# Kernel tuning notes

Hardware: AMD Instinct MI355X
Metric: run time of the kernel (lower is better)

The kernel has to match this reference:

```python
import jax, jax.numpy as jnp
import numpy as np

B, V, K, DIN, H, DH, OBS, HID = 2048, 3, 32, 256, 8, 64, 128, 256
REP = H * DH
EPS = 1e-6


def _ln(x, g, b):
    mu = x.mean(-1, keepdims=True)
    var = ((x - mu) ** 2).mean(-1, keepdims=True)
    return (x - mu) * jax.lax.rsqrt(var + 1e-5) * g + b


def setup_inputs() -> dict:
    key = jax.random.key(0)
    ks = iter(jax.random.split(key, 32))
    nrm = lambda shape, s=0.05: jax.random.normal(next(ks), shape, jnp.float32) * s
    return {
        'x_anchor': jax.random.normal(next(ks), (B, V, DIN), jnp.float32),
        'x_neighbors': jax.random.normal(next(ks), (B, V, K, DIN), jnp.float32),
        'edge_weights': jax.random.uniform(next(ks), (B, V, K), jnp.float32),
        'g': jax.random.normal(next(ks), (B, OBS), jnp.float32),
        'aW': nrm((V, DIN, REP)), 'ab': jnp.zeros((V, REP)), 'ag': jnp.ones((V, REP)), 'abeta': jnp.zeros((V, REP)),
        'nW': nrm((V, DIN, REP)), 'nb': jnp.zeros((V, REP)), 'ng': jnp.ones((V, REP)), 'nbeta': jnp.zeros((V, REP)),
        'Wq': nrm((V, H, DH, DH)), 'Wk': nrm((V, H, DH, DH)), 'Wv': nrm((V, H, DH, DH)), 'Wo': nrm((V, H, DH, DH)),
        'geom_log_scale': jnp.zeros((V, H)),
        'cWq': nrm((H, DH, DH)), 'cWk': nrm((H, DH, DH)), 'cWv': nrm((H, DH, DH)), 'cWo': nrm((H, DH, DH)),
        'rW1': nrm((OBS, HID)), 'rb1': jnp.zeros((HID,)),
        'rW2': nrm((HID, HID)), 'rb2': jnp.zeros((HID,)),
        'vW': nrm((HID, H * V)), 'vb': jnp.zeros((H * V,)),
        'mW': nrm((HID, H)), 'mb': jnp.zeros((H,)),
        'gW': nrm((HID, H)), 'gb': jnp.zeros((H,)),
    }


def reference(x_anchor, x_neighbors, edge_weights, g, aW, ab, ag, abeta, nW, nb, ng, nbeta,
              Wq, Wk, Wv, Wo, geom_log_scale, cWq, cWk, cWv, cWo,
              rW1, rb1, rW2, rb2, vW, vb, mW, mb, gW, gb):
    # --- per-view encoders (vectorized over V with a leading v axis) ---
    ha = _ln(jnp.einsum('bvi,vio->bvo', x_anchor, aW) + ab, ag, abeta).reshape(B, V, H, DH)
    hn = _ln(jnp.einsum('bvki,vio->bvko', x_neighbors, nW) + nb[:, None, :],
             ng[:, None, :], nbeta[:, None, :]).reshape(B, V, K, H, DH)
    q = jnp.einsum('bvhd,vhde->bvhe', ha, Wq)
    k = jnp.einsum('bvkhd,vhde->bvkhe', hn, Wk)
    vv = jnp.einsum('bvkhd,vhde->bvkhe', hn, Wv)
    sc = jnp.einsum('bvhd,bvkhd->bvhk', q, k) / np.sqrt(DH).astype(np.float32)
    geom = jax.nn.softplus(geom_log_scale)  # [V,H]
    sc = sc + geom[None, :, :, None] * jnp.log(edge_weights[:, :, None, :] + EPS)
    attn = jax.nn.softmax(sc, axis=-1)
    ho = jnp.einsum('bvhk,bvkhd->bvhd', attn, vv)
    ho = jnp.einsum('bvhd,vhde->bvhe', ho, Wo) + ha  # residual
    view_tokens = jnp.transpose(ho, (0, 2, 1, 3))  # [B,H,V,Dh]
    # --- router ---
    hid = jax.nn.gelu(jnp.dot(g, rW1) + rb1, approximate=False)
    hid = jax.nn.gelu(jnp.dot(hid, rW2) + rb2, approximate=False)
    pi = jax.nn.softmax((jnp.dot(hid, vW) + vb).reshape(B, H, V), axis=-1)
    beta = jax.nn.sigmoid((jnp.dot(hid, mW) + mb)[..., None])  # [B,H,1]
    gate = jax.nn.softmax(jnp.dot(hid, gW) + gb, axis=-1)      # [B,H]
    # --- pi-weighted mixture + cross-view interaction with log-pi prior ---
    mix = jnp.einsum('bhv,bhvd->bhd', pi, view_tokens)
    qc = jnp.einsum('bhd,hde->bhe', mix, cWq)
    kc = jnp.einsum('bhvd,hde->bhve', view_tokens, cWk)
    vc = jnp.einsum('bhvd,hde->bhve', view_tokens, cWv)
    s2 = jnp.einsum('bhd,bhvd->bhv', qc, kc) / np.sqrt(DH).astype(np.float32) + jnp.log(pi + EPS)
    a2 = jax.nn.softmax(s2, axis=-1)
    cr = jnp.einsum('bhv,bhvd->bhd', a2, vc)
    cr = jnp.einsum('bhd,hde->bhe', cr, cWo)
    # mode blend + head gating; head_repr kept unflattened [B,H,Dh]
    return gate[..., None] * (beta * cr + (1.0 - beta) * mix)
```

## Files before the change

### kernel.cpp

```cpp
#include <hip/hip_runtime.h>

#define B_   2048
#define V_   3
#define K_   32
#define DIN_ 256
#define H_   8
#define DH_  64
#define REP_ 512

typedef unsigned short u16;
typedef unsigned int   u32;
typedef __bf16 bf8 __attribute__((ext_vector_type(8)));
typedef float  f4  __attribute__((ext_vector_type(4)));

static __device__ __forceinline__ u16 f2bf(float f) {
  union { float f; u32 i; } x; x.f = f;
  u32 r = (x.i + 0x7FFFu + ((x.i >> 16) & 1u)) >> 16;
  return (u16)r;
}
static __device__ __forceinline__ float bf2f(u16 u) {
  union { u32 i; float f; } x; x.i = ((u32)u) << 16;
  return x.f;
}

static __device__ __forceinline__ void gl2lds16(const u16* g, u16* l) {
  __builtin_amdgcn_global_load_lds(
      (const __attribute__((address_space(1))) unsigned int*)(g),
      (__attribute__((address_space(3))) unsigned int*)(l), 16, 0, 0);
}
#define ASYNC_BARRIER() asm volatile("s_waitcnt vmcnt(0)\n\ts_barrier" ::: "memory")

__global__ __launch_bounds__(256) void k0_prep(
    const float* __restrict__ nW, const float* __restrict__ aW,
    const float* __restrict__ Wk, const float* __restrict__ Wv,
    u16* __restrict__ nWt, u16* __restrict__ aWt,
    u16* __restrict__ Wkt, u16* __restrict__ Wvt)
{
  int id = blockIdx.x * 256 + threadIdx.x;
  if (id < 393216) {
    int v  = id / 131072, r  = id % 131072;
    int kt = r / 16384,   r2 = r % 16384;
    int n  = r2 >> 5;
    int s  = (r2 >> 3) & 3;
    int m  = r2 & 7;
    int c  = s ^ ((n >> 1) & 3);
    int k  = kt * 32 + c * 8 + m;
    int src = (v * 256 + k) * 512 + n;
    nWt[id] = f2bf(nW[src]);
    aWt[id] = f2bf(aW[src]);
  } else {
    int j = id - 393216;
    int vh = j / 4096, r = j % 4096;
    int e = r / 64, d = r % 64;
    int src = (vh * 64 + d) * 64 + e;
    Wkt[j] = f2bf(Wk[src]);
    Wvt[j] = f2bf(Wv[src]);
  }
}

__global__ __launch_bounds__(256, 2) void k1_gemm_ln(
    const float* __restrict__ X,
    const u16*   __restrict__ Wt,
    const float* __restrict__ bias,
    const float* __restrict__ gamma,
    const float* __restrict__ betap,
    u16*   __restrict__ hn,
    float* __restrict__ ha,
    int mode, int b0, int Bc)
{
  __shared__ u16 sA[32 * 256];
  __shared__ u16 sB[2][16384];
  const int v = blockIdx.y, blk = blockIdx.x, t = threadIdx.x;
  const int w = t >> 6, l = t & 63, lm = l & 15, lg = l >> 4;

  float bcol[8];
  #pragma unroll
  for (int tn = 0; tn < 8; ++tn) bcol[tn] = bias[v * 512 + w * 128 + tn * 16 + lm];

  {
    int row = t >> 3;
    int cbase = (t & 7) * 32;
    long grow;
    if (mode == 0) { int b = b0 + blk; grow = ((long)(b * 3 + v) * 32 + row) * 256; }
    else           { int b = blk * 32 + row; grow = (long)(b * 3 + v) * 256; }
    const float4* src = (const float4*)(X + grow + cbase);
    int sw = row & 7;
    #pragma unroll
    for (int j = 0; j < 8; ++j) {
      float4 f = src[j];
      int col = cbase + j * 4;
      int c = col >> 3, m = col & 7;
      ushort4 u;
      u.x = f2bf(f.x); u.y = f2bf(f.y); u.z = f2bf(f.z); u.w = f2bf(f.w);
      *(ushort4*)&sA[row * 256 + ((c ^ sw) << 3) + m] = u;
    }
  }

  const u16* Wbase = Wt + (long)v * 8 * 16384;
  {
    const u16* gp = Wbase + w * 4096 + l * 8;
    u16* lp = &sB[0][w * 4096];
    #pragma unroll
    for (int j = 0; j < 8; ++j) gl2lds16(gp + j * 512, lp + j * 512);
  }
  __syncthreads();

  f4 acc[2][8];
  #pragma unroll
  for (int i = 0; i < 2; ++i)
    #pragma unroll
    for (int j = 0; j < 8; ++j) { f4 z = {0.f, 0.f, 0.f, 0.f}; acc[i][j] = z; }

  #pragma unroll
  for (int kt = 0; kt < 8; ++kt) {
    if (kt < 7) {
      const u16* gp = Wbase + (kt + 1) * 16384 + w * 4096 + l * 8;
      u16* lp = &sB[(kt + 1) & 1][w * 4096];
      #pragma unroll
      for (int j = 0; j < 8; ++j) gl2lds16(gp + j * 512, lp + j * 512);
    }
    const u16* Bcur = &sB[kt & 1][0];
    bf8 af[2];
    #pragma unroll
    for (int tm = 0; tm < 2; ++tm) {
      int row = tm * 16 + lm;
      int c = kt * 4 + lg;
      af[tm] = *(const bf8*)&sA[row * 256 + ((c ^ (row & 7)) << 3)];
    }
    #pragma unroll
    for (int tn = 0; tn < 8; ++tn) {
      int n = w * 128 + tn * 16 + lm;
      bf8 bv = *(const bf8*)&Bcur[n * 32 + ((lg ^ ((n >> 1) & 3)) << 3)];
      acc[0][tn] = __builtin_amdgcn_mfma_f32_16x16x32_bf16(af[0], bv, acc[0][tn], 0, 0, 0);
      acc[1][tn] = __builtin_amdgcn_mfma_f32_16x16x32_bf16(af[1], bv, acc[1][tn], 0, 0, 0);
    }
    if (kt < 7) ASYNC_BARRIER();
  }
  __syncthreads();

  u16* S = &sB[0][0];
  #pragma unroll
  for (int tm = 0; tm < 2; ++tm)
    #pragma unroll
    for (int tn = 0; tn < 8; ++tn) {
      int col = w * 128 + tn * 16 + lm;
      int c = col >> 3, m = col & 7;
      #pragma unroll
      for (int r = 0; r < 4; ++r) {
        int row = tm * 16 + lg * 4 + r;
        S[row * 512 + ((c ^ (row & 7)) << 3) + m] = f2bf(acc[tm][tn][r] + bcol[tn]);
      }
    }
  __syncthreads();

  {
    int row = t >> 3, ch = t & 7, sw = row & 7;
    float s1 = 0.f, s2 = 0.f;
    #pragma unroll
    for (int j = 0; j < 8; ++j) {
      int c = j * 8 + ch;
      const u16* p8 = &S[row * 512 + ((c ^ sw) << 3)];
      #pragma unroll
      for (int m = 0; m < 8; ++m) { float x = bf2f(p8[m]); s1 += x; s2 += x * x; }
    }
    #pragma unroll
    for (int d = 1; d < 8; d <<= 1) { s1 += __shfl_xor(s1, d, 64); s2 += __shfl_xor(s2, d, 64); }
    float mu = s1 * (1.f / 512.f);
    float var = s2 * (1.f / 512.f) - mu * mu;
    float rs = rsqrtf(var + 1e-5f);
    #pragma unroll
    for (int j = 0; j < 8; ++j) {
      int c = j * 8 + ch;
      const u16* p8 = &S[row * 512 + ((c ^ sw) << 3)];
      int col0 = c * 8;
      float4 g0 = *(const float4*)&gamma[v * 512 + col0];
      float4 g1 = *(const float4*)&gamma[v * 512 + col0 + 4];
      float4 e0 = *(const float4*)&betap[v * 512 + col0];
      float4 e1 = *(const float4*)&betap[v * 512 + col0 + 4];
      float y0 = (bf2f(p8[0]) - mu) * rs * g0.x + e0.x;
      float y1 = (bf2f(p8[1]) - mu) * rs * g0.y + e0.y;
      float y2 = (bf2f(p8[2]) - mu) * rs * g0.z + e0.z;
      float y3 = (bf2f(p8[3]) - mu) * rs * g0.w + e0.w;
      float y4 = (bf2f(p8[4]) - mu) * rs * g1.x + e1.x;
      float y5 = (bf2f(p8[5]) - mu) * rs * g1.y + e1.y;
      float y6 = (bf2f(p8[6]) - mu) * rs * g1.z + e1.z;
      float y7 = (bf2f(p8[7]) - mu) * rs * g1.w + e1.w;
      if (mode == 0) {
        uint4 q4;
        q4.x = (u32)f2bf(y0) | ((u32)f2bf(y1) << 16);
        q4.y = (u32)f2bf(y2) | ((u32)f2bf(y3) << 16);
        q4.z = (u32)f2bf(y4) | ((u32)f2bf(y5) << 16);
        q4.w = (u32)f2bf(y6) | ((u32)f2bf(y7) << 16);
        u16* dst = hn + (((long)(v * 8 + j) * Bc + blk) * 32 + row) * 64 + ch * 8;
        *(uint4*)dst = q4;
      } else {
        int b = blk * 32 + row;
        float* dst = ha + (long)(b * 3 + v) * 512 + col0;
        float4 w0, w1;
        w0.x = y0; w0.y = y1; w0.z = y2; w0.w = y3;
        w1.x = y4; w1.y = y5; w1.z = y6; w1.w = y7;
        *(float4*)dst = w0;
        *(float4*)(dst + 4) = w1;
      }
    }
  }
}

__global__ __launch_bounds__(256, 2) void k2_attn(
    const u16*   __restrict__ hn,
    const float* __restrict__ ha,
    const u16*   __restrict__ Wkt,
    const u16*   __restrict__ Wvt,
    const float* __restrict__ Wq,
    const float* __restrict__ Wo,
    const float* __restrict__ ew,
    const float* __restrict__ gls,
    float* __restrict__ vt,
    int b0, int Bc)
{
  const int v = blockIdx.z, h = blockIdx.y;
  const int bL0 = blockIdx.x * 4;
  const int t = threadIdx.x;
  __shared__ u16 A[128 * 72];
  __shared__ u16 Wk_s[64 * 72], Wv_s[64 * 72];
  __shared__ float q_s[4 * 64], ha_s[4 * 64], attn_s[4 * 32], o_s[4 * 64];

  {
    const uint4* src = (const uint4*)(hn + ((long)(v * 8 + h) * Bc + bL0) * 2048);
    int r = t >> 1, half = t & 1;
    #pragma unroll
    for (int i = 0; i < 4; ++i) {
      uint4 d = src[r * 8 + half * 4 + i];
      *(uint4*)&A[r * 72 + half * 32 + i * 8] = d;
    }
  }
  {
    const uint4* sk = (const uint4*)(Wkt + (long)(v * 8 + h) * 4096);
    const uint4* sv = (const uint4*)(Wvt + (long)(v * 8 + h) * 4096);
    #pragma unroll
    for (int i = 0; i < 2; ++i) {
      int idx = i * 256 + t;
      int n = idx >> 3, k8 = (idx & 7) * 8;
      *(uint4*)&Wk_s[n * 72 + k8] = sk[idx];
      *(uint4*)&Wv_s[n * 72 + k8] = sv[idx];
    }
  }
  {
    int b = t >> 6, e = t & 63;
    ha_s[t] = ha[((long)(b0 + bL0 + b) * 3 + v) * 512 + h * 64 + e];
  }
  __syncthreads();

  const int w = t >> 6, l = t & 63, lm = l & 15, lg = l >> 4;
  f4 aK[2][4], aV[2][4];
  #pragma unroll
  for (int i = 0; i < 2; ++i)
    #pragma unroll
    for (int j = 0; j < 4; ++j) { f4 z = {0.f, 0.f, 0.f, 0.f}; aK[i][j] = z; aV[i][j] = z; }

  #pragma unroll
  for (int ks = 0; ks < 2; ++ks) {
    int ko = ks * 32 + lg * 8;
    bf8 af[2];
    #pragma unroll
    for (int tm = 0; tm < 2; ++tm) af[tm] = *(const bf8*)&A[(w * 32 + tm * 16 + lm) * 72 + ko];
    #pragma unroll
    for (int tn = 0; tn < 4; ++tn) {
      bf8 bk = *(const bf8*)&Wk_s[(tn * 16 + lm) * 72 + ko];
      bf8 bv = *(const bf8*)&Wv_s[(tn * 16 + lm) * 72 + ko];
      #pragma unroll
      for (int tm = 0; tm < 2; ++tm) {
        aK[tm][tn] = __builtin_amdgcn_mfma_f32_16x16x32_bf16(af[tm], bk, aK[tm][tn], 0, 0, 0);
        aV[tm][tn] = __builtin_amdgcn_mfma_f32_16x16x32_bf16(af[tm], bv, aV[tm][tn], 0, 0, 0);
      }
    }
  }
  __syncthreads();

  #pragma unroll
  for (int tm = 0; tm < 2; ++tm)
    #pragma unroll
    for (int tn = 0; tn < 4; ++tn)
      #pragma unroll
      for (int r = 0; r < 4; ++r) {
        int row = w * 32 + tm * 16 + lg * 4 + r;
        int col = tn * 16 + lm;
        A[row * 72 + col] = f2bf(aK[tm][tn][r]);
      }
  {
    const float* wq = Wq + (long)(v * 8 + h) * 4096;
    int b = t >> 6, e = t & 63;
    float acc = 0.f;
    for (int d = 0; d < 64; ++d) acc += ha_s[b * 64 + d] * wq[d * 64 + e];
    q_s[t] = acc * 0.125f;
  }
  __syncthreads();

  if (t < 128) {
    int b = t >> 5, k = t & 31;
    float x = gls[v * 8 + h];
    float gsc = (x > 20.f) ? x : log1pf(expf(x));
    float s = 0.f;
    const u16* kr = &A[(b * 32 + k) * 72];
    for (int d = 0; d < 64; ++d) s += q_s[b * 64 + d] * bf2f(kr[d]);
    float e_w = ew[((long)(b0 + bL0 + b) * 3 + v) * 32 + k];
    s += gsc * logf(e_w + 1e-6f);
    float m = s;
    #pragma unroll
    for (int d = 1; d < 32; d <<= 1) m = fmaxf(m, __shfl_xor(m, d, 64));
    float exs = expf(s - m), sum = exs;
    #pragma unroll
    for (int d = 1; d < 32; d <<= 1) sum += __shfl_xor(sum, d, 64);
    attn_s[b * 32 + k] = exs / sum;
  }
  __syncthreads();

  {
    float p[4] = {0.f, 0.f, 0.f, 0.f};
    #pragma unroll
    for (int tm = 0; tm < 2; ++tm)
      #pragma unroll
      for (int r = 0; r < 4; ++r) {
        int k = tm * 16 + lg * 4 + r;
        float a = attn_s[w * 32 + k];
        #pragma unroll
        for (int tn = 0; tn < 4; ++tn) p[tn] += a * aV[tm][tn][r];
      }
    #pragma unroll
    for (int tn = 0; tn < 4; ++tn) {
      float x = p[tn];
      x += __shfl_xor(x, 16, 64);
      x += __shfl_xor(x, 32, 64);
      if (l < 16) o_s[w * 64 + tn * 16 + lm] = x;
    }
  }
  __syncthreads();

  {
    const float* wo = Wo + (long)(v * 8 + h) * 4096;
    int b = t >> 6, e = t & 63;
    float acc = ha_s[b * 64 + e];
    for (int d = 0; d < 64; ++d) acc += o_s[b * 64 + d] * wo[d * 64 + e];
    vt[(((long)(b0 + bL0 + b) * 8 + h) * 3 + v) * 64 + e] = acc;
  }
}

__global__ __launch_bounds__(256) void k3_router(
    const float* __restrict__ g, const float* __restrict__ rW1, const float* __restrict__ rb1,
    const float* __restrict__ rW2, const float* __restrict__ rb2,
    const float* __restrict__ vW, const float* __restrict__ vb,
    const float* __restrict__ mW, const float* __restrict__ mb,
    const float* __restrict__ gW, const float* __restrict__ gb,
    float* __restrict__ pi, float* __restrict__ beta_o, float* __restrict__ gate_o)
{
  __shared__ float gs[4 * 128], h1[4 * 256], h2[4 * 256], lgt[4 * 40];
  int t = threadIdx.x, bb = blockIdx.x * 4;
  #pragma unroll
  for (int r = 0; r < 2; ++r) { int idx = r * 256 + t; gs[idx] = g[(long)bb * 128 + idx]; }
  __syncthreads();
  {
    int bl = t >> 6, e0 = (t & 63) * 4;
    float acc[4];
    #pragma unroll
    for (int j = 0; j < 4; ++j) acc[j] = rb1[e0 + j];
    for (int i = 0; i < 128; ++i) {
      float gv = gs[bl * 128 + i];
      const float* wr = rW1 + i * 256 + e0;
      #pragma unroll
      for (int j = 0; j < 4; ++j) acc[j] += gv * wr[j];
    }
    #pragma unroll
    for (int j = 0; j < 4; ++j) { float x = acc[j]; h1[bl * 256 + e0 + j] = 0.5f * x * (1.f + erff(x * 0.70710678118f)); }
  }
  __syncthreads();
  {
    int bl = t >> 6, e0 = (t & 63) * 4;
    float acc[4];
    #pragma unroll
    for (int j = 0; j < 4; ++j) acc[j] = rb2[e0 + j];
    for (int i = 0; i < 256; ++i) {
      float hv = h1[bl * 256 + i];
      const float* wr = rW2 + i * 256 + e0;
      #pragma unroll
      for (int j = 0; j < 4; ++j) acc[j] += hv * wr[j];
    }
    #pragma unroll
    for (int j = 0; j < 4; ++j) { float x = acc[j]; h2[bl * 256 + e0 + j] = 0.5f * x * (1.f + erff(x * 0.70710678118f)); }
  }
  __syncthreads();
  if (t < 160) {
    int bl = t / 40, j = t % 40;
    const float* W; float bs; int col, stride;
    if (j < 24)      { W = vW; col = j;      stride = 24; bs = vb[j]; }
    else if (j < 32) { W = mW; col = j - 24; stride = 8;  bs = mb[j - 24]; }
    else             { W = gW; col = j - 32; stride = 8;  bs = gb[j - 32]; }
    float acc = bs;
    for (int i = 0; i < 256; ++i) acc += h2[bl * 256 + i] * W[i * stride + col];
    lgt[bl * 40 + j] = acc;
  }
  __syncthreads();
  if (t < 4) {
    int b = bb + t;
    const float* L = &lgt[t * 40];
    #pragma unroll
    for (int hh = 0; hh < 8; ++hh) {
      float a0 = L[hh * 3], a1 = L[hh * 3 + 1], a2v = L[hh * 3 + 2];
      float m = fmaxf(a0, fmaxf(a1, a2v));
      float x0 = expf(a0 - m), x1 = expf(a1 - m), x2 = expf(a2v - m);
      float inv = 1.f / (x0 + x1 + x2);
      pi[b * 24 + hh * 3 + 0] = x0 * inv;
      pi[b * 24 + hh * 3 + 1] = x1 * inv;
      pi[b * 24 + hh * 3 + 2] = x2 * inv;
      beta_o[b * 8 + hh] = 1.f / (1.f + expf(-L[24 + hh]));
    }
    float m = L[32];
    #pragma unroll
    for (int hh = 1; hh < 8; ++hh) m = fmaxf(m, L[32 + hh]);
    float s = 0.f, ex[8];
    #pragma unroll
    for (int hh = 0; hh < 8; ++hh) { ex[hh] = expf(L[32 + hh] - m); s += ex[hh]; }
    float inv = 1.f / s;
    #pragma unroll
    for (int hh = 0; hh < 8; ++hh) gate_o[b * 8 + hh] = ex[hh] * inv;
  }
}

__global__ __launch_bounds__(256) void k4_cross(
    const float* __restrict__ vtg, const float* __restrict__ pig,
    const float* __restrict__ betag, const float* __restrict__ gateg,
    const float* __restrict__ cWq, const float* __restrict__ cWk,
    const float* __restrict__ cWv, const float* __restrict__ cWo,
    float* __restrict__ out)
{
  __shared__ float smem[12544];
  float* vts   = smem;
  float* mixs  = smem + 6144;
  float* buf1  = smem + 8192;
  float* buf2  = smem + 10240;
  float* a2s   = smem + 12288;
  float* pis   = smem + 12384;
  float* betas = smem + 12480;
  float* gates = smem + 12512;

  int t = threadIdx.x, bblk = blockIdx.x * 4;
  {
    const float4* src = (const float4*)(vtg + (long)bblk * 1536);
    #pragma unroll
    for (int r = 0; r < 6; ++r) ((float4*)vts)[r * 256 + t] = src[r * 256 + t];
    if (t < 96) pis[t] = pig[bblk * 24 + t];
    if (t < 32) { betas[t] = betag[bblk * 8 + t]; gates[t] = gateg[bblk * 8 + t]; }
  }
  __syncthreads();
  int bl = t >> 6, hh = (t >> 3) & 7, e0 = (t & 7) * 8;
  const float* vbh = &vts[(bl * 8 + hh) * 192];
  {
    float p0 = pis[bl * 24 + hh * 3], p1 = pis[bl * 24 + hh * 3 + 1], p2 = pis[bl * 24 + hh * 3 + 2];
    #pragma unroll
    for (int j = 0; j < 8; ++j) {
      int e = e0 + j;
      mixs[(bl * 8 + hh) * 64 + e] = p0 * vbh[e] + p1 * vbh[64 + e] + p2 * vbh[128 + e];
    }
  }
  __syncthreads();
  {
    float acc[8] = {0.f,0.f,0.f,0.f,0.f,0.f,0.f,0.f};
    const float* M = &mixs[(bl * 8 + hh) * 64];
    for (int d = 0; d < 64; ++d) {
      float mv = M[d];
      const float* wr = &cWq[(hh * 64 + d) * 64 + e0];
      #pragma unroll
      for (int j = 0; j < 8; ++j) acc[j] += mv * wr[j];
    }
    #pragma unroll
    for (int j = 0; j < 8; ++j) buf1[(bl * 8 + hh) * 64 + e0 + j] = acc[j] * 0.125f;
  }
  __syncthreads();
  {
    const float* Q = &buf1[(bl * 8 + hh) * 64];
    #pragma unroll
    for (int d2 = 0; d2 < 8; ++d2) {
      const float* wr = &cWk[(hh * 64 + e0 + d2) * 64];
      float a = 0.f;
      for (int e = 0; e < 64; ++e) a += wr[e] * Q[e];
      buf2[(bl * 8 + hh) * 64 + e0 + d2] = a;
    }
  }
  __syncthreads();
  if (t < 32) {
    int b2 = t >> 3, h2 = t & 7;
    const float* Wd = &buf2[(b2 * 8 + h2) * 64];
    const float* vb2 = &vts[(b2 * 8 + h2) * 192];
    float s[3];
    #pragma unroll
    for (int v3 = 0; v3 < 3; ++v3) {
      float a = 0.f;
      for (int d = 0; d < 64; ++d) a += Wd[d] * vb2[v3 * 64 + d];
      s[v3] = a + logf(pis[b2 * 24 + h2 * 3 + v3] + 1e-6f);
    }
    float m = fmaxf(s[0], fmaxf(s[1], s[2]));
    float x0 = expf(s[0] - m), x1 = expf(s[1] - m), x2 = expf(s[2] - m);
    float inv = 1.f / (x0 + x1 + x2);
    a2s[(b2 * 8 + h2) * 3 + 0] = x0 * inv;
    a2s[(b2 * 8 + h2) * 3 + 1] = x1 * inv;
    a2s[(b2 * 8 + h2) * 3 + 2] = x2 * inv;
  }
  __syncthreads();
  {
    float a0 = a2s[(bl * 8 + hh) * 3], a1 = a2s[(bl * 8 + hh) * 3 + 1], a2v = a2s[(bl * 8 + hh) * 3 + 2];
    #pragma unroll
    for (int j = 0; j < 8; ++j) {
      int e = e0 + j;
      buf1[(bl * 8 + hh) * 64 + e] = a0 * vbh[e] + a1 * vbh[64 + e] + a2v * vbh[128 + e];
    }
  }
  __syncthreads();
  {
    float acc[8] = {0.f,0.f,0.f,0.f,0.f,0.f,0.f,0.f};
    const float* Y = &buf1[(bl * 8 + hh) * 64];
    for (int d = 0; d < 64; ++d) {
      float yv = Y[d];
      const float* wr = &cWv[(hh * 64 + d) * 64 + e0];
      #pragma unroll
      for (int j = 0; j < 8; ++j) acc[j] += yv * wr[j];
    }
    #pragma unroll
    for (int j = 0; j < 8; ++j) buf2[(bl * 8 + hh) * 64 + e0 + j] = acc[j];
  }
  __syncthreads();
  {
    float acc[8] = {0.f,0.f,0.f,0.f,0.f,0.f,0.f,0.f};
    const float* C2 = &buf2[(bl * 8 + hh) * 64];
    for (int d = 0; d < 64; ++d) {
      float cv = C2[d];
      const float* wr = &cWo[(hh * 64 + d) * 64 + e0];
      #pragma unroll
      for (int j = 0; j < 8; ++j) acc[j] += cv * wr[j];
    }
    float bt = betas[bl * 8 + hh], gt = gates[bl * 8 + hh];
    const float* M = &mixs[(bl * 8 + hh) * 64];
    #pragma unroll
    for (int j = 0; j < 8; ++j)
      out[((long)(bblk + bl) * 8 + hh) * 64 + e0 + j] = gt * (bt * acc[j] + (1.f - bt) * M[e0 + j]);
  }
}

extern "C" void kernel_launch(void* const* d_in, const int* in_sizes, int n_in,
                              void* d_out, int out_size, void* d_ws, size_t ws_size,
                              hipStream_t stream) {
  const float* x_anchor    = (const float*)d_in[0];
  const float* x_neighbors = (const float*)d_in[1];
  const float* edge_w      = (const float*)d_in[2];
  const float* g           = (const float*)d_in[3];
  const float* aW  = (const float*)d_in[4];
  const float* ab  = (const float*)d_in[5];
  const float* ag  = (const float*)d_in[6];
  const float* abeta = (const float*)d_in[7];
  const float* nW  = (const float*)d_in[8];
  const float* nb  = (const float*)d_in[9];
  const float* ng  = (const float*)d_in[10];
  const float* nbeta = (const float*)d_in[11];
  const float* Wq  = (const float*)d_in[12];
  const float* Wk  = (const float*)d_in[13];
  const float* Wv  = (const float*)d_in[14];
  const float* Wo  = (const float*)d_in[15];
  const float* gls = (const float*)d_in[16];
  const float* cWq = (const float*)d_in[17];
  const float* cWk = (const float*)d_in[18];
  const float* cWv = (const float*)d_in[19];
  const float* cWo = (const float*)d_in[20];
  const float* rW1 = (const float*)d_in[21];
  const float* rb1 = (const float*)d_in[22];
  const float* rW2 = (const float*)d_in[23];
  const float* rb2 = (const float*)d_in[24];
  const float* vW  = (const float*)d_in[25];
  const float* vb  = (const float*)d_in[26];
  const float* mW  = (const float*)d_in[27];
  const float* mb  = (const float*)d_in[28];
  const float* gW  = (const float*)d_in[29];
  const float* gb  = (const float*)d_in[30];

  char* p = (char*)d_ws;
  u16* nWt = (u16*)p;  p += 786432;
  u16* aWt = (u16*)p;  p += 786432;
  u16* Wkt = (u16*)p;  p += 196608;
  u16* Wvt = (u16*)p;  p += 196608;
  float* ha   = (float*)p; p += 12582912;
  float* vtb  = (float*)p; p += 12582912;
  float* pib  = (float*)p; p += 196608;
  float* betb = (float*)p; p += 65536;
  float* gatb = (float*)p; p += 65536;
  size_t fixed = (size_t)(p - (char*)d_ws);
  int C = 1;
  while (C < 128 && fixed + (size_t)(2048 / C) * 98304 > ws_size) C <<= 1;
  int Bc = 2048 / C;
  u16* hnb = (u16*)p;

  k0_prep<<<1920, 256, 0, stream>>>(nW, aW, Wk, Wv, nWt, aWt, Wkt, Wvt);
  k1_gemm_ln<<<dim3(64, 3), 256, 0, stream>>>(x_anchor, aWt, ab, ag, abeta,
                                              (u16*)nullptr, ha, 1, 0, Bc);
  k3_router<<<512, 256, 0, stream>>>(g, rW1, rb1, rW2, rb2, vW, vb, mW, mb, gW, gb,
                                     pib, betb, gatb);
  for (int c = 0; c < C; ++c) {
    int b0 = c * Bc;
    k1_gemm_ln<<<dim3(Bc, 3), 256, 0, stream>>>(x_neighbors, nWt, nb, ng, nbeta,
                                                hnb, (float*)nullptr, 0, b0, Bc);
    k2_attn<<<dim3(Bc / 4, 8, 3), 256, 0, stream>>>(hnb, ha, Wkt, Wvt, Wq, Wo,
                                                    edge_w, gls, vtb, b0, Bc);
  }
  k4_cross<<<512, 256, 0, stream>>>(vtb, pib, betb, gatb, cWq, cWk, cWv, cWo,
                                    (float*)d_out);
}
```

Baseline: 784.7 us.

## Fold Wq·Wk^T into one matrix, enlarge GEMM-LN tile to 64 rows

Precomputes Wqk = Wq·Wk^T per view-head, so attention scores come from ha·Wqk dotted directly with hn. This removes the K projection MFMAs, the LDS round trip of K, and the Wk staging in the attention kernel. The neighbor GEMM+LayerNorm kernel now runs 512 threads per block over 64 rows, reusing each weight tile across twice as many rows, but it drops the double-buffered async weight prefetch for a single buffer with two barriers per k-step. The LN and score loops also read bf16 values as packed 128-bit words.

Result: faster. 748.6 us (-4.6%).

```diff
diff --git a/kernel.cpp b/kernel.cpp
--- a/kernel.cpp
+++ b/kernel.cpp
@@ -22,19 +22,24 @@
   union { u32 i; float f; } x; x.i = ((u32)u) << 16;
   return x.f;
 }
+static __device__ __forceinline__ float bflo(u32 q) {
+  union { u32 i; float f; } x; x.i = q << 16; return x.f;
+}
+static __device__ __forceinline__ float bfhi(u32 q) {
+  union { u32 i; float f; } x; x.i = q & 0xffff0000u; return x.f;
+}
 
 static __device__ __forceinline__ void gl2lds16(const u16* g, u16* l) {
   __builtin_amdgcn_global_load_lds(
       (const __attribute__((address_space(1))) unsigned int*)(g),
       (__attribute__((address_space(3))) unsigned int*)(l), 16, 0, 0);
 }
-#define ASYNC_BARRIER() asm volatile("s_waitcnt vmcnt(0)\n\ts_barrier" ::: "memory")
 
 __global__ __launch_bounds__(256) void k0_prep(
     const float* __restrict__ nW, const float* __restrict__ aW,
-    const float* __restrict__ Wk, const float* __restrict__ Wv,
+    const float* __restrict__ Wv,
     u16* __restrict__ nWt, u16* __restrict__ aWt,
-    u16* __restrict__ Wkt, u16* __restrict__ Wvt)
+    u16* __restrict__ Wvt)
 {
   int id = blockIdx.x * 256 + threadIdx.x;
   if (id < 393216) {
@@ -53,12 +58,44 @@
     int vh = j / 4096, r = j % 4096;
     int e = r / 64, d = r % 64;
     int src = (vh * 64 + d) * 64 + e;
-    Wkt[j] = f2bf(Wk[src]);
     Wvt[j] = f2bf(Wv[src]);
   }
 }
 
-__global__ __launch_bounds__(256, 2) void k1_gemm_ln(
+__global__ __launch_bounds__(256) void k0_wqk(
+    const float* __restrict__ Wq, const float* __restrict__ Wk,
+    float* __restrict__ Wqk)
+{
+  int vh = blockIdx.x, t = threadIdx.x;
+  __shared__ float wq[4096], wkT[4096];
+  #pragma unroll
+  for (int i = 0; i < 16; ++i) {
+    int idx = i * 256 + t;
+    wq[idx] = Wq[(long)vh * 4096 + idx];
+    int e = idx >> 6, c = idx & 63;
+    wkT[c * 64 + e] = Wk[(long)vh * 4096 + e * 64 + c];
+  }
+  __syncthreads();
+  int d = t >> 2, e0 = (t & 3) * 16;
+  float acc[16];
+  #pragma unroll
+  for (int j = 0; j < 16; ++j) acc[j] = 0.f;
+  for (int c = 0; c < 64; ++c) {
+    float a = wq[d * 64 + c];
+    const float* wr = &wkT[c * 64 + e0];
+    #pragma unroll
+    for (int j = 0; j < 16; ++j) acc[j] += a * wr[j];
+  }
+  #pragma unroll
+  for (int j = 0; j < 16; ++j) Wqk[(long)vh * 4096 + d * 64 + e0 + j] = acc[j];
+}
+
+union K1Smem {
+  struct { u16 A[64 * 256]; u16 B[16384]; } p;
+  u16 S[64 * 512];
+};
+
+__global__ __launch_bounds__(512, 4) void k1_gemm_ln(
     const float* __restrict__ X,
     const u16*   __restrict__ Wt,
     const float* __restrict__ bias,
@@ -68,21 +105,21 @@
     float* __restrict__ ha,
     int mode, int b0, int Bc)
 {
-  __shared__ u16 sA[32 * 256];
-  __shared__ u16 sB[2][16384];
+  __shared__ K1Smem sm;
   const int v = blockIdx.y, blk = blockIdx.x, t = threadIdx.x;
   const int w = t >> 6, l = t & 63, lm = l & 15, lg = l >> 4;
+  const int wm = w & 1, wn = w >> 1;
 
   float bcol[8];
   #pragma unroll
-  for (int tn = 0; tn < 8; ++tn) bcol[tn] = bias[v * 512 + w * 128 + tn * 16 + lm];
+  for (int tn = 0; tn < 8; ++tn) bcol[tn] = bias[v * 512 + wn * 128 + tn * 16 + lm];
 
   {
     int row = t >> 3;
     int cbase = (t & 7) * 32;
     long grow;
-    if (mode == 0) { int b = b0 + blk; grow = ((long)(b * 3 + v) * 32 + row) * 256; }
-    else           { int b = blk * 32 + row; grow = (long)(b * 3 + v) * 256; }
+    if (mode == 0) { int b = b0 + blk * 2 + (row >> 5); grow = ((long)(b * 3 + v) * 32 + (row & 31)) * 256; }
+    else           { int b = blk * 64 + row;            grow = (long)(b * 3 + v) * 256; }
     const float4* src = (const float4*)(X + grow + cbase);
     int sw = row & 7;
     #pragma unroll
@@ -92,63 +129,53 @@
       int c = col >> 3, m = col & 7;
       ushort4 u;
       u.x = f2bf(f.x); u.y = f2bf(f.y); u.z = f2bf(f.z); u.w = f2bf(f.w);
-      *(ushort4*)&sA[row * 256 + ((c ^ sw) << 3) + m] = u;
-    }
-  }
+      *(ushort4*)&sm.p.A[row * 256 + ((c ^ sw) << 3) + m] = u;
+    }
+  }
+
+  f4 acc[2][8];
+  #pragma unroll
+  for (int i = 0; i < 2; ++i)
+    #pragma unroll
+    for (int j = 0; j < 8; ++j) { f4 z = {0.f, 0.f, 0.f, 0.f}; acc[i][j] = z; }
 
   const u16* Wbase = Wt + (long)v * 8 * 16384;
-  {
-    const u16* gp = Wbase + w * 4096 + l * 8;
-    u16* lp = &sB[0][w * 4096];
-    #pragma unroll
-    for (int j = 0; j < 8; ++j) gl2lds16(gp + j * 512, lp + j * 512);
-  }
-  __syncthreads();
-
-  f4 acc[2][8];
-  #pragma unroll
-  for (int i = 0; i < 2; ++i)
-    #pragma unroll
-    for (int j = 0; j < 8; ++j) { f4 z = {0.f, 0.f, 0.f, 0.f}; acc[i][j] = z; }
-
-  #pragma unroll
   for (int kt = 0; kt < 8; ++kt) {
-    if (kt < 7) {
-      const u16* gp = Wbase + (kt + 1) * 16384 + w * 4096 + l * 8;
-      u16* lp = &sB[(kt + 1) & 1][w * 4096];
-      #pragma unroll
-      for (int j = 0; j < 8; ++j) gl2lds16(gp + j * 512, lp + j * 512);
-    }
-    const u16* Bcur = &sB[kt & 1][0];
+    __syncthreads();
+    {
+      const u16* gp = Wbase + (long)kt * 16384 + t * 8;
+      u16* lp = &sm.p.B[t * 8];
+      #pragma unroll
+      for (int r = 0; r < 4; ++r) gl2lds16(gp + r * 4096, lp + r * 4096);
+    }
+    __syncthreads();
     bf8 af[2];
     #pragma unroll
     for (int tm = 0; tm < 2; ++tm) {
-      int row = tm * 16 + lm;
+      int row = wm * 32 + tm * 16 + lm;
       int c = kt * 4 + lg;
-      af[tm] = *(const bf8*)&sA[row * 256 + ((c ^ (row & 7)) << 3)];
+      af[tm] = *(const bf8*)&sm.p.A[row * 256 + ((c ^ (row & 7)) << 3)];
     }
     #pragma unroll
     for (int tn = 0; tn < 8; ++tn) {
-      int n = w * 128 + tn * 16 + lm;
-      bf8 bv = *(const bf8*)&Bcur[n * 32 + ((lg ^ ((n >> 1) & 3)) << 3)];
+      int n = wn * 128 + tn * 16 + lm;
+      bf8 bv = *(const bf8*)&sm.p.B[n * 32 + ((lg ^ ((n >> 1) & 3)) << 3)];
       acc[0][tn] = __builtin_amdgcn_mfma_f32_16x16x32_bf16(af[0], bv, acc[0][tn], 0, 0, 0);
       acc[1][tn] = __builtin_amdgcn_mfma_f32_16x16x32_bf16(af[1], bv, acc[1][tn], 0, 0, 0);
     }
-    if (kt < 7) ASYNC_BARRIER();
-  }
-  __syncthreads();
-
-  u16* S = &sB[0][0];
+  }
+  __syncthreads();
+
   #pragma unroll
   for (int tm = 0; tm < 2; ++tm)
     #pragma unroll
     for (int tn = 0; tn < 8; ++tn) {
-      int col = w * 128 + tn * 16 + lm;
+      int col = wn * 128 + tn * 16 + lm;
       int c = col >> 3, m = col & 7;
       #pragma unroll
       for (int r = 0; r < 4; ++r) {
-        int row = tm * 16 + lg * 4 + r;
-        S[row * 512 + ((c ^ (row & 7)) << 3) + m] = f2bf(acc[tm][tn][r] + bcol[tn]);
+        int row = wm * 32 + tm * 16 + lg * 4 + r;
+        sm.S[row * 512 + ((c ^ (row & 7)) << 3) + m] = f2bf(acc[tm][tn][r] + bcol[tn]);
       }
     }
   __syncthreads();
@@ -159,9 +186,11 @@
     #pragma unroll
     for (int j = 0; j < 8; ++j) {
       int c = j * 8 + ch;
-      const u16* p8 = &S[row * 512 + ((c ^ sw) << 3)];
-      #pragma unroll
-      for (int m = 0; m < 8; ++m) { float x = bf2f(p8[m]); s1 += x; s2 += x * x; }
+      uint4 q = *(const uint4*)&sm.S[row * 512 + ((c ^ sw) << 3)];
+      float x0 = bflo(q.x), x1 = bfhi(q.x), x2 = bflo(q.y), x3 = bfhi(q.y);
+      float x4 = bflo(q.z), x5 = bfhi(q.z), x6 = bflo(q.w), x7 = bfhi(q.w);
+      s1 += ((x0 + x1) + (x2 + x3)) + ((x4 + x5) + (x6 + x7));
+      s2 += ((x0*x0 + x1*x1) + (x2*x2 + x3*x3)) + ((x4*x4 + x5*x5) + (x6*x6 + x7*x7));
     }
     #pragma unroll
     for (int d = 1; d < 8; d <<= 1) { s1 += __shfl_xor(s1, d, 64); s2 += __shfl_xor(s2, d, 64); }
@@ -171,30 +200,31 @@
     #pragma unroll
     for (int j = 0; j < 8; ++j) {
       int c = j * 8 + ch;
-      const u16* p8 = &S[row * 512 + ((c ^ sw) << 3)];
+      uint4 q = *(const uint4*)&sm.S[row * 512 + ((c ^ sw) << 3)];
       int col0 = c * 8;
       float4 g0 = *(const float4*)&gamma[v * 512 + col0];
       float4 g1 = *(const float4*)&gamma[v * 512 + col0 + 4];
       float4 e0 = *(const float4*)&betap[v * 512 + col0];
       float4 e1 = *(const float4*)&betap[v * 512 + col0 + 4];
-      float y0 = (bf2f(p8[0]) - mu) * rs * g0.x + e0.x;
-      float y1 = (bf2f(p8[1]) - mu) * rs * g0.y + e0.y;
-      float y2 = (bf2f(p8[2]) - mu) * rs * g0.z + e0.z;
-      float y3 = (bf2f(p8[3]) - mu) * rs * g0.w + e0.w;
-      float y4 = (bf2f(p8[4]) - mu) * rs * g1.x + e1.x;
-      float y5 = (bf2f(p8[5]) - mu) * rs * g1.y + e1.y;
-      float y6 = (bf2f(p8[6]) - mu) * rs * g1.z + e1.z;
-      float y7 = (bf2f(p8[7]) - mu) * rs * g1.w + e1.w;
+      float y0 = (bflo(q.x) - mu) * rs * g0.x + e0.x;
+      float y1 = (bfhi(q.x) - mu) * rs * g0.y + e0.y;
+      float y2 = (bflo(q.y) - mu) * rs * g0.z + e0.z;
+      float y3 = (bfhi(q.y) - mu) * rs * g0.w + e0.w;
+      float y4 = (bflo(q.z) - mu) * rs * g1.x + e1.x;
+      float y5 = (bfhi(q.z) - mu) * rs * g1.y + e1.y;
+      float y6 = (bflo(q.w) - mu) * rs * g1.z + e1.z;
+      float y7 = (bfhi(q.w) - mu) * rs * g1.w + e1.w;
       if (mode == 0) {
         uint4 q4;
         q4.x = (u32)f2bf(y0) | ((u32)f2bf(y1) << 16);
         q4.y = (u32)f2bf(y2) | ((u32)f2bf(y3) << 16);
         q4.z = (u32)f2bf(y4) | ((u32)f2bf(y5) << 16);
         q4.w = (u32)f2bf(y6) | ((u32)f2bf(y7) << 16);
-        u16* dst = hn + (((long)(v * 8 + j) * Bc + blk) * 32 + row) * 64 + ch * 8;
+        int bl_ = blk * 2 + (row >> 5), krow = row & 31;
+        u16* dst = hn + (((long)(v * 8 + j) * Bc + bl_) * 32 + krow) * 64 + ch * 8;
         *(uint4*)dst = q4;
       } else {
-        int b = blk * 32 + row;
+        int b = blk * 64 + row;
         float* dst = ha + (long)(b * 3 + v) * 512 + col0;
         float4 w0, w1;
         w0.x = y0; w0.y = y1; w0.z = y2; w0.w = y3;
@@ -209,9 +239,8 @@
 __global__ __launch_bounds__(256, 2) void k2_attn(
     const u16*   __restrict__ hn,
     const float* __restrict__ ha,
-    const u16*   __restrict__ Wkt,
     const u16*   __restrict__ Wvt,
-    const float* __restrict__ Wq,
+    const float* __restrict__ Wqk,
     const float* __restrict__ Wo,
     const float* __restrict__ ew,
     const float* __restrict__ gls,
@@ -222,8 +251,8 @@
   const int bL0 = blockIdx.x * 4;
   const int t = threadIdx.x;
   __shared__ u16 A[128 * 72];
-  __shared__ u16 Wk_s[64 * 72], Wv_s[64 * 72];
-  __shared__ float q_s[4 * 64], ha_s[4 * 64], attn_s[4 * 32], o_s[4 * 64];
+  __shared__ u16 Wv_s[64 * 72];
+  __shared__ float t_s[4 * 64], ha_s[4 * 64], attn_s[4 * 32], o_s[4 * 64];
 
   {
     const uint4* src = (const uint4*)(hn + ((long)(v * 8 + h) * Bc + bL0) * 2048);
@@ -235,13 +264,11 @@
     }
   }
   {
-    const uint4* sk = (const uint4*)(Wkt + (long)(v * 8 + h) * 4096);
     const uint4* sv = (const uint4*)(Wvt + (long)(v * 8 + h) * 4096);
     #pragma unroll
     for (int i = 0; i < 2; ++i) {
       int idx = i * 256 + t;
       int n = idx >> 3, k8 = (idx & 7) * 8;
-      *(uint4*)&Wk_s[n * 72 + k8] = sk[idx];
       *(uint4*)&Wv_s[n * 72 + k8] = sv[idx];
     }
   }
@@ -252,11 +279,11 @@
   __syncthreads();
 
   const int w = t >> 6, l = t & 63, lm = l & 15, lg = l >> 4;
-  f4 aK[2][4], aV[2][4];
+  f4 aV[2][4];
   #pragma unroll
   for (int i = 0; i < 2; ++i)
     #pragma unroll
-    for (int j = 0; j < 4; ++j) { f4 z = {0.f, 0.f, 0.f, 0.f}; aK[i][j] = z; aV[i][j] = z; }
+    for (int j = 0; j < 4; ++j) { f4 z = {0.f, 0.f, 0.f, 0.f}; aV[i][j] = z; }
 
   #pragma unroll
   for (int ks = 0; ks < 2; ++ks) {
@@ -266,33 +293,19 @@
     for (int tm = 0; tm < 2; ++tm) af[tm] = *(const bf8*)&A[(w * 32 + tm * 16 + lm) * 72 + ko];
     #pragma unroll
     for (int tn = 0; tn < 4; ++tn) {
-      bf8 bk = *(const bf8*)&Wk_s[(tn * 16 + lm) * 72 + ko];
       bf8 bv = *(const bf8*)&Wv_s[(tn * 16 + lm) * 72 + ko];
       #pragma unroll
-      for (int tm = 0; tm < 2; ++tm) {
-        aK[tm][tn] = __builtin_amdgcn_mfma_f32_16x16x32_bf16(af[tm], bk, aK[tm][tn], 0, 0, 0);
+      for (int tm = 0; tm < 2; ++tm)
         aV[tm][tn] = __builtin_amdgcn_mfma_f32_16x16x32_bf16(af[tm], bv, aV[tm][tn], 0, 0, 0);
-      }
-    }
-  }
-  __syncthreads();
-
-  #pragma unroll
-  for (int tm = 0; tm < 2; ++tm)
-    #pragma unroll
-    for (int tn = 0; tn < 4; ++tn)
-      #pragma unroll
-      for (int r = 0; r < 4; ++r) {
-        int row = w * 32 + tm * 16 + lg * 4 + r;
-        int col = tn * 16 + lm;
-        A[row * 72 + col] = f2bf(aK[tm][tn][r]);
-      }
-  {
-    const float* wq = Wq + (long)(v * 8 + h) * 4096;
+    }
+  }
+
+  {
+    const float* wqk = Wqk + (long)(v * 8 + h) * 4096;
     int b = t >> 6, e = t & 63;
     float acc = 0.f;
-    for (int d = 0; d < 64; ++d) acc += ha_s[b * 64 + d] * wq[d * 64 + e];
-    q_s[t] = acc * 0.125f;
+    for (int d = 0; d < 64; ++d) acc += ha_s[b * 64 + d] * wqk[d * 64 + e];
+    t_s[t] = acc * 0.125f;
   }
   __syncthreads();
 
@@ -302,7 +315,16 @@
     float gsc = (x > 20.f) ? x : log1pf(expf(x));
     float s = 0.f;
     const u16* kr = &A[(b * 32 + k) * 72];
-    for (int d = 0; d < 64; ++d) s += q_s[b * 64 + d] * bf2f(kr[d]);
+    const float* tb = &t_s[b * 64];
+    #pragma unroll
+    for (int j = 0; j < 8; ++j) {
+      uint4 q = *(const uint4*)(kr + j * 8);
+      const float* tj = tb + j * 8;
+      s += tj[0] * bflo(q.x) + tj[1] * bfhi(q.x)
+         + tj[2] * bflo(q.y) + tj[3] * bfhi(q.y)
+         + tj[4] * bflo(q.z) + tj[5] * bfhi(q.z)
+         + tj[6] * bflo(q.w) + tj[7] * bfhi(q.w);
+    }
     float e_w = ew[((long)(b0 + bL0 + b) * 3 + v) * 32 + k];
     s += gsc * logf(e_w + 1e-6f);
     float m = s;
@@ -582,8 +604,8 @@
   char* p = (char*)d_ws;
   u16* nWt = (u16*)p;  p += 786432;
   u16* aWt = (u16*)p;  p += 786432;
-  u16* Wkt = (u16*)p;  p += 196608;
   u16* Wvt = (u16*)p;  p += 196608;
+  float* WqkB = (float*)p; p += 393216;
   float* ha   = (float*)p; p += 12582912;
   float* vtb  = (float*)p; p += 12582912;
   float* pib  = (float*)p; p += 196608;
@@ -595,16 +617,17 @@
   int Bc = 2048 / C;
   u16* hnb = (u16*)p;
 
-  k0_prep<<<1920, 256, 0, stream>>>(nW, aW, Wk, Wv, nWt, aWt, Wkt, Wvt);
-  k1_gemm_ln<<<dim3(64, 3), 256, 0, stream>>>(x_anchor, aWt, ab, ag, abeta,
+  k0_prep<<<1920, 256, 0, stream>>>(nW, aW, Wv, nWt, aWt, Wvt);
+  k0_wqk<<<24, 256, 0, stream>>>(Wq, Wk, WqkB);
+  k1_gemm_ln<<<dim3(32, 3), 512, 0, stream>>>(x_anchor, aWt, ab, ag, abeta,
                                               (u16*)nullptr, ha, 1, 0, Bc);
   k3_router<<<512, 256, 0, stream>>>(g, rW1, rb1, rW2, rb2, vW, vb, mW, mb, gW, gb,
                                      pib, betb, gatb);
   for (int c = 0; c < C; ++c) {
     int b0 = c * Bc;
-    k1_gemm_ln<<<dim3(Bc, 3), 256, 0, stream>>>(x_neighbors, nWt, nb, ng, nbeta,
-                                                hnb, (float*)nullptr, 0, b0, Bc);
-    k2_attn<<<dim3(Bc / 4, 8, 3), 256, 0, stream>>>(hnb, ha, Wkt, Wvt, Wq, Wo,
+    k1_gemm_ln<<<dim3(Bc / 2, 3), 512, 0, stream>>>(x_neighbors, nWt, nb, ng, nbeta,
+                                                    hnb, (float*)nullptr, 0, b0, Bc);
+    k2_attn<<<dim3(Bc / 4, 8, 3), 256, 0, stream>>>(hnb, ha, Wvt, WqkB, Wo,
                                                     edge_w, gls, vtb, b0, Bc);
   }
   k4_cross<<<512, 256, 0, stream>>>(vtb, pib, betb, gatb, cWq, cWk, cWv, cWo,
```
